# Kernel tuning notes

Measured on AMD Instinct MI355X. Metric: run time of the kernel, lower is better.

## Reference

```python
import jax, jax.numpy as jnp
import numpy as np

INNER_DIM = 256
DT_SIZE = 64
STATE_DIM = 256  # must equal INNER_DIM for the original split() to be valid
BATCH, SEQ_LEN = 2, 512


def setup_inputs() -> dict:
    key = jax.random.key(0)
    k_x, k_win, k_wdt, k_bdt = jax.random.split(key, 4)
    x = jax.random.normal(k_x, (BATCH, SEQ_LEN, INNER_DIM), dtype=jnp.float32)
    # nn.Linear(inner_dim, dt_size + 2*state_dim, bias=False); stored as [in, out] for x @ W
    W_in = jax.random.normal(k_win, (INNER_DIM, DT_SIZE + 2 * STATE_DIM), dtype=jnp.float32) / np.sqrt(INNER_DIM)
    # nn.Linear(dt_size, inner_dim) with bias
    W_dt = jax.random.normal(k_wdt, (DT_SIZE, INNER_DIM), dtype=jnp.float32) / np.sqrt(DT_SIZE)
    b_dt = jax.random.normal(k_bdt, (INNER_DIM,), dtype=jnp.float32) * 0.01
    # alpha_log = log(repeat(arange(1, N+1), 'n -> d n'))
    alpha_log = jnp.log(jnp.broadcast_to(
        jnp.arange(1, STATE_DIM + 1, dtype=jnp.float32), (INNER_DIM, STATE_DIM)))
    delta = jnp.ones((INNER_DIM,), dtype=jnp.float32)
    return {"input_tensor": x, "W_in": W_in, "W_dt": W_dt, "b_dt": b_dt,
            "alpha_log": alpha_log, "delta": delta}


def reference(input_tensor, W_in, W_dt, b_dt, alpha_log, delta):
    x = input_tensor
    alpha = -jnp.exp(alpha_log)  # [D, N]
    proj = x @ W_in  # [B, L, DT + 2D]
    dt_raw, beta, gamma = jnp.split(proj, [DT_SIZE, DT_SIZE + INNER_DIM], axis=-1)
    dt = jax.nn.softplus(dt_raw @ W_dt + b_dt)  # [B, L, D]
    # dt_a = exp(dt[...,None] * alpha) : [B, L, D, N]
    dt_a = jnp.exp(jnp.einsum('bld,dn->bldn', dt, alpha))
    # dt_b_i = dt * x outer beta : [B, L, D, N]
    dt_b_i = jnp.einsum('bld,bln->bldn', dt * x, beta)

    def step(state, inputs):
        a_t, b_t, g_t = inputs  # [B,D,N], [B,D,N], [B,N]
        state = a_t * state + b_t
        y_t = jnp.einsum('bdn,bn->bd', state, g_t)
        return state, y_t

    s0 = jnp.zeros((x.shape[0], INNER_DIM, STATE_DIM), dtype=x.dtype)
    _, ys = jax.lax.scan(step, s0, (jnp.moveaxis(dt_a, 1, 0),
                                    jnp.moveaxis(dt_b_i, 1, 0),
                                    jnp.moveaxis(gamma, 1, 0)))
    ys = jnp.moveaxis(ys, 0, 1)  # [B, L, D]
    return ys + x * delta
```

## Files before the change

kernel.cpp:

```cpp
#include <hip/hip_runtime.h>
#include <math.h>

#define DIM   256
#define NST   256
#define LSEQ  512
#define BAT   2
#define DTSZ  64
#define PCOLS 576
#define NROWS 1024

constexpr float LOG2E = 1.4426950408889634f;

__device__ __forceinline__ float fexp2(float v) {
#if __has_builtin(__builtin_amdgcn_exp2f)
    return __builtin_amdgcn_exp2f(v);
#else
    return exp2f(v);
#endif
}

__device__ __forceinline__ float softplusf(float v) {
    return (v > 20.f) ? v : log1pf(__expf(v));
}

__device__ __forceinline__ void barrier_lds_only() {
    __builtin_amdgcn_s_waitcnt(0xC07F);
    __builtin_amdgcn_s_barrier();
}

__device__ __forceinline__ unsigned pack_bg(float be, float ga) {
    unsigned ub = __float_as_uint(be);
    unsigned ug = __float_as_uint(ga);
    ub = (ub + 0x7fffu + ((ub >> 16) & 1u)) >> 16;
    ug = (ug + 0x7fffu + ((ug >> 16) & 1u)) & 0xffff0000u;
    return ub | ug;
}

__global__ __launch_bounds__(256, 2) void proj_kernel(
    const float* __restrict__ x, const float* __restrict__ W_in,
    const float* __restrict__ W_dt, const float* __restrict__ b_dt,
    unsigned* __restrict__ betgam,
    float* __restrict__ dtp, float* __restrict__ dtxp)
{
    __shared__ float xs[2][DIM];
    __shared__ float draw[2][DTSZ];
    const int j = threadIdx.x;
    const int row0 = blockIdx.x * 2;

    #pragma unroll
    for (int r = 0; r < 2; ++r) xs[r][j] = x[(row0 + r) * DIM + j];
    __syncthreads();

    float acc0[2] = {0.f, 0.f}, acc1[2] = {0.f, 0.f}, acc2[2] = {0.f, 0.f};
    const bool has2 = (j < 64);

    for (int kk = 0; kk < DIM; kk += 16) {
        float w0[16], w1[16], w2[16];
        #pragma unroll
        for (int u = 0; u < 16; ++u) {
            const int k = kk + u;
            w0[u] = W_in[k * PCOLS + j];
            w1[u] = W_in[k * PCOLS + 256 + j];
            w2[u] = has2 ? W_in[k * PCOLS + 512 + j] : 0.f;
        }
        #pragma unroll
        for (int r = 0; r < 2; ++r) {
            #pragma unroll
            for (int q = 0; q < 4; ++q) {
                float4 xv = *(const float4*)&xs[r][kk + q * 4];
                const float xa[4] = {xv.x, xv.y, xv.z, xv.w};
                #pragma unroll
                for (int u = 0; u < 4; ++u) {
                    const int uu = q * 4 + u;
                    acc0[r] = fmaf(xa[u], w0[uu], acc0[r]);
                    acc1[r] = fmaf(xa[u], w1[uu], acc1[r]);
                    acc2[r] = fmaf(xa[u], w2[uu], acc2[r]);
                }
            }
        }
    }

    #pragma unroll
    for (int r = 0; r < 2; ++r) {
        const int row = row0 + r;
        if (has2) {
            draw[r][j] = acc0[r];
            betgam[row * NST + 192 + j] = pack_bg(acc1[r], acc2[r]);
        } else {
            betgam[row * NST + (j - 64)] = pack_bg(acc0[r], acc1[r]);
        }
    }
    __syncthreads();

    float bd = b_dt[j];
    float accd[2] = {bd, bd};
    #pragma unroll 16
    for (int k = 0; k < DTSZ; ++k) {
        float w = W_dt[k * DIM + j];
        #pragma unroll
        for (int r = 0; r < 2; ++r) accd[r] = fmaf(draw[r][k], w, accd[r]);
    }
    #pragma unroll
    for (int r = 0; r < 2; ++r) {
        const int row = row0 + r;
        float sp = softplusf(accd[r]);
        dtp[row * DIM + j]  = sp;
        dtxp[row * DIM + j] = sp * xs[r][j];
    }
}

__global__ __launch_bounds__(256, 2) void scan1p(
    const float* __restrict__ x,
    const float* __restrict__ alpha_log,
    const float* __restrict__ delta,
    const unsigned* __restrict__ betgam,
    const float* __restrict__ dtp,
    const float* __restrict__ dtxp,
    float* __restrict__ out)
{
    __shared__ float part[32][NST];
    __shared__ float dts[LSEQ], dxs[LSEQ], xcol[LSEQ];
    const int n = threadIdx.x;
    const int xcd  = blockIdx.x & 7;
    const int slot = blockIdx.x >> 3;
    const int b = xcd >> 2;
    const int d = slot * 4 + (xcd & 3);
    const int rb = b * LSEQ;

    #pragma unroll
    for (int it = 0; it < 2; ++it) {
        const int l = n + it * 256;
        dts[l]  = dtp [(rb + l) * DIM + d];
        dxs[l]  = dtxp[(rb + l) * DIM + d];
        xcol[l] = x   [(rb + l) * DIM + d];
    }
    const float aln = -__expf(alpha_log[d * NST + n]) * LOG2E;
    const float dv  = delta[d];
    __syncthreads();

    float s = 0.f;
    unsigned bg[8][8];
    #pragma unroll
    for (int pw = 0; pw < 6; ++pw) {
        #pragma unroll
        for (int t = 0; t < 8; ++t)
            bg[pw][t] = betgam[(rb + pw * 8 + t) * NST + n];
    }

    #pragma unroll 8
    for (int w = 0; w < 64; ++w) {
        const int cur = w & 7;
        const int pf  = (w + 6) & 7;
        if (w + 6 < 64) {
            #pragma unroll
            for (int t = 0; t < 8; ++t)
                bg[pf][t] = betgam[(rb + (w + 6) * 8 + t) * NST + n];
        }
        float4 dta = *(const float4*)&dts[w * 8];
        float4 dtb = *(const float4*)&dts[w * 8 + 4];
        float4 dxa = *(const float4*)&dxs[w * 8];
        float4 dxb = *(const float4*)&dxs[w * 8 + 4];
        const float dtw[8] = {dta.x, dta.y, dta.z, dta.w, dtb.x, dtb.y, dtb.z, dtb.w};
        const float dxw[8] = {dxa.x, dxa.y, dxa.z, dxa.w, dxb.x, dxb.y, dxb.z, dxb.w};

        const int prow = (w & 3) * 8;
        #pragma unroll
        for (int t = 0; t < 8; ++t) {
            const unsigned u = bg[cur][t];
            const float be = __uint_as_float(u << 16);
            const float ga = __uint_as_float(u & 0xffff0000u);
            float a = fexp2(dtw[t] * aln);
            s = fmaf(a, s, dxw[t] * be);
            part[prow + t][n] = s * ga;
        }

        if ((w & 3) == 3) {
            barrier_lds_only();
            const int trow = n >> 3, seg = n & 7;
            float sum = 0.f;
            #pragma unroll
            for (int k = 0; k < 32; ++k)
                sum += part[trow][seg * 32 + ((k + n) & 31)];
            sum += __shfl_xor(sum, 1);
            sum += __shfl_xor(sum, 2);
            sum += __shfl_xor(sum, 4);
            if (seg == 0) {
                const int l = (w >> 2) * 32 + trow;
                out[(rb + l) * DIM + d] = sum + xcol[l] * dv;
            }
            barrier_lds_only();
        }
    }
}

extern "C" void kernel_launch(void* const* d_in, const int* in_sizes, int n_in,
                              void* d_out, int out_size, void* d_ws, size_t ws_size,
                              hipStream_t stream) {
    const float* x         = (const float*)d_in[0];
    const float* W_in      = (const float*)d_in[1];
    const float* W_dt      = (const float*)d_in[2];
    const float* b_dt      = (const float*)d_in[3];
    const float* alpha_log = (const float*)d_in[4];
    const float* delta     = (const float*)d_in[5];
    float* out = (float*)d_out;

    unsigned* betgam = (unsigned*)d_ws;
    float* dtp  = (float*)(betgam + NROWS * NST);
    float* dtxp = dtp + NROWS * DIM;

    proj_kernel<<<NROWS / 2, 256, 0, stream>>>(x, W_in, W_dt, b_dt, betgam, dtp, dtxp);
    scan1p<<<BAT * DIM, 256, 0, stream>>>(x, alpha_log, delta, betgam, dtp, dtxp, out);
}
```

Measured before the change: 119.2 us.

## Restructure projection kernel: one thread per output column, 4 rows per block, readlane broadcasts

```diff
diff --git a/kernel.cpp b/kernel.cpp
--- a/kernel.cpp
+++ b/kernel.cpp
@@ -36,76 +36,79 @@
     return ub | ug;
 }
 
-__global__ __launch_bounds__(256, 2) void proj_kernel(
+__device__ __forceinline__ float rdlane(float v, int l) {
+    return __uint_as_float((unsigned)__builtin_amdgcn_readlane(
+        (int)__float_as_uint(v), l));
+}
+
+__global__ __launch_bounds__(576) void proj_kernel(
     const float* __restrict__ x, const float* __restrict__ W_in,
     const float* __restrict__ W_dt, const float* __restrict__ b_dt,
     unsigned* __restrict__ betgam,
     float* __restrict__ dtp, float* __restrict__ dtxp)
 {
-    __shared__ float xs[2][DIM];
-    __shared__ float draw[2][DTSZ];
-    const int j = threadIdx.x;
-    const int row0 = blockIdx.x * 2;
-
-    #pragma unroll
-    for (int r = 0; r < 2; ++r) xs[r][j] = x[(row0 + r) * DIM + j];
+    __shared__ float Ls[4][PCOLS];
+    const int tid  = threadIdx.x;
+    const int lane = tid & 63;
+    const int r0   = blockIdx.x * 4;
+
+    float vA[4][4];
+    #pragma unroll
+    for (int r = 0; r < 4; ++r) {
+        #pragma unroll
+        for (int q = 0; q < 4; ++q)
+            vA[r][q] = x[(r0 + r) * DIM + q * 64 + lane];
+    }
+
+    float acc[4] = {0.f, 0.f, 0.f, 0.f};
+    const float* wp = W_in + tid;
+    #pragma unroll
+    for (int q = 0; q < 4; ++q) {
+        #pragma unroll 8
+        for (int kl = 0; kl < 64; ++kl) {
+            const float bw = wp[(q * 64 + kl) * PCOLS];
+            #pragma unroll
+            for (int r = 0; r < 4; ++r)
+                acc[r] = fmaf(rdlane(vA[r][q], kl), bw, acc[r]);
+        }
+    }
+
+    #pragma unroll
+    for (int r = 0; r < 4; ++r) Ls[r][tid] = acc[r];
     __syncthreads();
 
-    float acc0[2] = {0.f, 0.f}, acc1[2] = {0.f, 0.f}, acc2[2] = {0.f, 0.f};
-    const bool has2 = (j < 64);
-
-    for (int kk = 0; kk < DIM; kk += 16) {
-        float w0[16], w1[16], w2[16];
-        #pragma unroll
-        for (int u = 0; u < 16; ++u) {
-            const int k = kk + u;
-            w0[u] = W_in[k * PCOLS + j];
-            w1[u] = W_in[k * PCOLS + 256 + j];
-            w2[u] = has2 ? W_in[k * PCOLS + 512 + j] : 0.f;
-        }
-        #pragma unroll
-        for (int r = 0; r < 2; ++r) {
-            #pragma unroll
-            for (int q = 0; q < 4; ++q) {
-                float4 xv = *(const float4*)&xs[r][kk + q * 4];
-                const float xa[4] = {xv.x, xv.y, xv.z, xv.w};
-                #pragma unroll
-                for (int u = 0; u < 4; ++u) {
-                    const int uu = q * 4 + u;
-                    acc0[r] = fmaf(xa[u], w0[uu], acc0[r]);
-                    acc1[r] = fmaf(xa[u], w1[uu], acc1[r]);
-                    acc2[r] = fmaf(xa[u], w2[uu], acc2[r]);
-                }
-            }
-        }
-    }
-
-    #pragma unroll
-    for (int r = 0; r < 2; ++r) {
-        const int row = row0 + r;
-        if (has2) {
-            draw[r][j] = acc0[r];
-            betgam[row * NST + 192 + j] = pack_bg(acc1[r], acc2[r]);
-        } else {
-            betgam[row * NST + (j - 64)] = pack_bg(acc0[r], acc1[r]);
-        }
-    }
-    __syncthreads();
-
-    float bd = b_dt[j];
-    float accd[2] = {bd, bd};
-    #pragma unroll 16
-    for (int k = 0; k < DTSZ; ++k) {
-        float w = W_dt[k * DIM + j];
-        #pragma unroll
-        for (int r = 0; r < 2; ++r) accd[r] = fmaf(draw[r][k], w, accd[r]);
-    }
-    #pragma unroll
-    for (int r = 0; r < 2; ++r) {
-        const int row = row0 + r;
-        float sp = softplusf(accd[r]);
-        dtp[row * DIM + j]  = sp;
-        dtxp[row * DIM + j] = sp * xs[r][j];
+    if (tid < 256) {
+        const int d = tid;
+        float vD[4];
+        #pragma unroll
+        for (int r = 0; r < 4; ++r) vD[r] = Ls[r][lane];
+
+        const float bd = b_dt[d];
+        float accd[4] = {bd, bd, bd, bd};
+        const float* wdp = W_dt + d;
+        #pragma unroll 8
+        for (int k = 0; k < DTSZ; ++k) {
+            const float wv = wdp[k * DIM];
+            #pragma unroll
+            for (int r = 0; r < 4; ++r)
+                accd[r] = fmaf(rdlane(vD[r], k), wv, accd[r]);
+        }
+        #pragma unroll
+        for (int r = 0; r < 4; ++r) {
+            const int row = r0 + r;
+            const float sp = softplusf(accd[r]);
+            const float xv = x[row * DIM + d];
+            dtp[row * DIM + d]  = sp;
+            dtxp[row * DIM + d] = sp * xv;
+        }
+    } else if (tid < 512) {
+        const int n = tid - 256;
+        #pragma unroll
+        for (int r = 0; r < 4; ++r) {
+            const float be = Ls[r][64 + n];
+            const float ga = Ls[r][320 + n];
+            betgam[(r0 + r) * NST + n] = pack_bg(be, ga);
+        }
     }
 }
 
@@ -208,6 +211,6 @@
     float* dtp  = (float*)(betgam + NROWS * NST);
     float* dtxp = dtp + NROWS * DIM;
 
-    proj_kernel<<<NROWS / 2, 256, 0, stream>>>(x, W_in, W_dt, b_dt, betgam, dtp, dtxp);
+    proj_kernel<<<NROWS / 4, 576, 0, stream>>>(x, W_in, W_dt, b_dt, betgam, dtp, dtxp);
     scan1p<<<BAT * DIM, 256, 0, stream>>>(x, alpha_log, delta, betgam, dtp, dtxp, out);
 }
```

Result: slower. 122.1 us (+2.4%).
